# Optimization experiments

Hardware: AMD Instinct MI355X
Metric: run time of the kernel (lower is better)

The kernel has to match this reference:

```python
import jax, jax.numpy as jnp
import numpy as np

D_IN, D_OUT, K = 128, 128, 64
X_MIN, X_MAX = 0.0, 1.0
EPS = 1e-12


def _pchip_slopes(y, x):
    # y: [..., K], x: [K] strictly increasing -> slopes [..., K]. Assumes K >= 3.
    h = x[1:] - x[:-1]                      # [K-1]
    delta = (y[..., 1:] - y[..., :-1]) / (h + EPS)
    h0, h1 = h[:-1], h[1:]
    w1 = 2.0 * h1 + h0
    w2 = h1 + 2.0 * h0
    d0_, d1_ = delta[..., :-1], delta[..., 1:]
    same_sign = d0_ * d1_ > 0
    denom = w1 / (d0_ + EPS) + w2 / (d1_ + EPS)
    d_int = jnp.where(same_sign, (w1 + w2) / (denom + EPS), 0.0)  # [..., K-2]
    d_first = ((2.0 * h[0] + h[1]) * delta[..., 0] - h[0] * delta[..., 1]) / (h[0] + h[1] + EPS)
    d_last = ((2.0 * h[-1] + h[-2]) * delta[..., -1] - h[-1] * delta[..., -2]) / (h[-1] + h[-2] + EPS)

    def limit(di, de):
        di = jnp.where(di * de <= 0, 0.0, di)
        return jnp.where(jnp.abs(di) > 3.0 * jnp.abs(de), 3.0 * de, di)

    d_first = limit(d_first, delta[..., 0])
    d_last = limit(d_last, delta[..., -1])
    return jnp.concatenate([d_first[..., None], d_int, d_last[..., None]], axis=-1)


def setup_inputs() -> dict:
    key = jax.random.key(0)
    k1, k2 = jax.random.split(key)
    x = jax.random.normal(k1, (4096, D_IN), dtype=jnp.float32)
    coeffs = 0.2 * jax.random.normal(k2, (D_OUT, D_IN, K), dtype=jnp.float32)
    bias = jnp.zeros((D_OUT,), dtype=jnp.float32)
    knots = jnp.linspace(X_MIN, X_MAX, K, dtype=jnp.float32)
    return {"x": x, "coeffs": coeffs, "bias": bias, "knots": knots}


def reference(x, coeffs, bias, knots):
    B = x.shape[0]
    slopes = _pchip_slopes(coeffs, knots)              # [d_out, d_in, K]
    h = (X_MAX - X_MIN) / (K - 1)

    xc = jnp.clip(x, X_MIN, X_MAX)                     # [B, d_in]
    idx = jnp.clip(jnp.floor((xc - X_MIN) / h).astype(jnp.int32), 0, K - 2)
    t = (xc - (X_MIN + idx.astype(x.dtype) * h)) / h   # [B, d_in]
    t2 = t * t
    t3 = t2 * t
    h00 = 2 * t3 - 3 * t2 + 1
    h10 = t3 - 2 * t2 + t
    h01 = -2 * t3 + 3 * t2
    h11 = t3 - t2

    ct = jnp.transpose(coeffs, (1, 2, 0))              # [d_in, K, d_out]
    dt = jnp.transpose(slopes, (1, 2, 0))              # [d_in, K, d_out]
    ii = jnp.arange(D_IN)[None, :]                     # [1, d_in]
    y0 = ct[ii, idx]                                   # [B, d_in, d_out]
    y1 = ct[ii, idx + 1]
    d0 = dt[ii, idx]
    d1 = dt[ii, idx + 1]

    yi = (h00[..., None] * y0 + h10[..., None] * h * d0
          + h01[..., None] * y1 + h11[..., None] * h * d1)  # [B, d_in, d_out]

    # linear extrapolation beyond the knot range
    y_left = ct[:, 0, :][None] + dt[:, 0, :][None] * (x - X_MIN)[..., None]
    y_right = ct[:, -1, :][None] + dt[:, -1, :][None] * (x - X_MAX)[..., None]
    yi = jnp.where((x < X_MIN)[..., None], y_left, yi)
    yi = jnp.where((x > X_MAX)[..., None], y_right, yi)

    return yi.sum(axis=1) + bias[None, :]              # [B, d_out]
```

## Files before the change

kernel.cpp:

```cpp
#include <hip/hip_runtime.h>

#define KN 64
#define DIN 128
#define DOUT 128
#define EPSF 1e-12f
#define HF (1.0f / 63.0f)

typedef _Float16 h2 __attribute__((ext_vector_type(2)));
typedef float    f2 __attribute__((ext_vector_type(2)));

#if defined(__has_builtin)
#if __has_builtin(__builtin_amdgcn_fdot2)
#define FDOT2(a, b, c) __builtin_amdgcn_fdot2((a), (b), (c), false)
#endif
#if __has_builtin(__builtin_amdgcn_cvt_pk_fp8_f32) && __has_builtin(__builtin_amdgcn_cvt_pk_f32_fp8)
#define HAVE_HW_FP8 1
#endif
#endif
#ifndef FDOT2
static __device__ __forceinline__ float FDOT2(h2 a, h2 b, float c) {
    return c + (float)a.x * (float)b.x + (float)a.y * (float)b.y;
}
#endif

#ifndef HAVE_HW_FP8
static __device__ __forceinline__ unsigned enc8(float x) {
    unsigned s = (x < 0.0f) ? 1u : 0u;
    x = fabsf(x);
    x = fminf(x, 448.0f);
    if (x < 0.015625f) {
        unsigned m = (unsigned)(x * 512.0f + 0.5f);
        return (s << 7) | m;
    }
    int e; float fr = frexpf(x, &e);
    int E = e - 1 + 7;
    unsigned m = (unsigned)((2.0f * fr - 1.0f) * 8.0f + 0.5f);
    if (m == 8) { m = 0; ++E; }
    if (E > 15) { E = 15; m = 6; }
    return (s << 7) | ((unsigned)E << 3) | m;
}
static __device__ __forceinline__ float dec8(unsigned b) {
    unsigned s = b >> 7, e = (b >> 3) & 15, m = b & 7;
    float v = (e == 0) ? ldexpf((float)m, -9) : ldexpf(8.0f + (float)m, (int)e - 10);
    return s ? -v : v;
}
#endif

static __device__ __forceinline__ unsigned pack4_fp8(float a, float b, float c, float d) {
#ifdef HAVE_HW_FP8
    int r = __builtin_amdgcn_cvt_pk_fp8_f32(a, b, 0, false);
    r = __builtin_amdgcn_cvt_pk_fp8_f32(c, d, r, true);
    return (unsigned)r;
#else
    return enc8(a) | (enc8(b) << 8) | (enc8(c) << 16) | (enc8(d) << 24);
#endif
}
static __device__ __forceinline__ f2 dec2lo(unsigned u) {
#ifdef HAVE_HW_FP8
    return __builtin_amdgcn_cvt_pk_f32_fp8((int)u, false);
#else
    f2 r; r.x = dec8(u & 255u); r.y = dec8((u >> 8) & 255u); return r;
#endif
}
static __device__ __forceinline__ f2 dec2hi(unsigned u) {
#ifdef HAVE_HW_FP8
    return __builtin_amdgcn_cvt_pk_f32_fp8((int)u, true);
#else
    f2 r; r.x = dec8((u >> 16) & 255u); r.y = dec8((u >> 24) & 255u); return r;
#endif
}

#define EXT_ELE (128 * 63 * 64)

__global__ __launch_bounds__(256) void kan_precompute(
    const float* __restrict__ coeffs,
    const float* __restrict__ knots,
    uint2* __restrict__ tb)
{
    const int i      = blockIdx.x >> 1;
    const int o_base = (blockIdx.x & 1) << 6;
    const int wave   = threadIdx.x >> 6;
    const int lane   = threadIdx.x & 63;

    __shared__ float ys[64][65];
    __shared__ float ds[64][65];

    float kn  = knots[lane];
    float kn1 = (lane < 63) ? knots[lane + 1] : 0.0f;
    float hk  = kn1 - kn;
    float hm1 = __shfl_up(hk, 1);
    float h1v = __shfl_down(hk, 1);
    float hm2 = __shfl_up(hk, 2);

    for (int ol = wave; ol < 64; ol += 4) {
        const int o = o_base + ol;
        float y = coeffs[(o * DIN + i) * KN + lane];
        float ynext = __shfl_down(y, 1);
        float delta = (lane < 63) ? (ynext - y) / (hk + EPSF) : 0.0f;
        float dm1 = __shfl_up(delta, 1);

        float w1v = 2.0f * hk + hm1;
        float w2v = hk + 2.0f * hm1;
        float denom = w1v / (dm1 + EPSF) + w2v / (delta + EPSF);
        float d = (dm1 * delta > 0.0f) ? (w1v + w2v) / (denom + EPSF) : 0.0f;

        float d1v = __shfl_down(delta, 1);
        if (lane == 0) {
            float df = ((2.0f * hk + h1v) * delta - hk * d1v) / (hk + h1v + EPSF);
            if (df * delta <= 0.0f) df = 0.0f;
            else if (fabsf(df) > 3.0f * fabsf(delta)) df = 3.0f * delta;
            d = df;
        }
        float dm2 = __shfl_up(delta, 2);
        if (lane == 63) {
            float dl = ((2.0f * hm1 + hm2) * dm1 - hm1 * dm2) / (hm1 + hm2 + EPSF);
            if (dl * dm1 <= 0.0f) dl = 0.0f;
            else if (fabsf(dl) > 3.0f * fabsf(dm1)) dl = 3.0f * dm1;
            d = dl;
        }
        ys[ol][lane] = y;
        ds[ol][lane] = d * HF;
    }
    __syncthreads();

    const int p  = threadIdx.x & 31;
    const int op = (o_base >> 1) + p;
    const int ol0 = p << 1;
    for (int j = threadIdx.x >> 5; j < 63; j += 8) {
        unsigned wa = pack4_fp8(ys[ol0][j],     ds[ol0][j],     ys[ol0][j + 1],     ds[ol0][j + 1]);
        unsigned wb = pack4_fp8(ys[ol0 + 1][j], ds[ol0 + 1][j], ys[ol0 + 1][j + 1], ds[ol0 + 1][j + 1]);
        uint2 v; v.x = wa; v.y = wb;
        tb[(i * 63 + j) * 64 + op] = v;
    }
    if (threadIdx.x < 64) {
        const int pp   = threadIdx.x & 31;
        const int side = threadIdx.x >> 5;
        const int k    = side ? 63 : 0;
        const int o0   = pp << 1;
        h2 ea; ea.x = (_Float16)ys[o0][k];     ea.y = (_Float16)ds[o0][k];
        h2 eb; eb.x = (_Float16)ys[o0 + 1][k]; eb.y = (_Float16)ds[o0 + 1][k];
        uint2 v;
        v.x = __builtin_bit_cast(unsigned int, ea);
        v.y = __builtin_bit_cast(unsigned int, eb);
        tb[EXT_ELE + (i * 2 + side) * 64 + (o_base >> 1) + pp] = v;
    }
}

__global__ __launch_bounds__(256) void kan_main(
    const float* __restrict__ x,
    const uint2* __restrict__ tb2,
    const float* __restrict__ bias,
    float* __restrict__ out)
{
    const int b0   = blockIdx.x << 1;
    const int tid  = threadIdx.x;
    const int wv   = tid >> 6;
    const int bl   = wv >> 1;
    const int half = wv & 1;
    const int lane = tid & 63;

    __shared__ uint4  wl[2][DIN];
    __shared__ float4 wlf[2][DIN];
    __shared__ float2 red[2][64];

    {
        const int bl1 = tid >> 7;
        const int i1  = tid & 127;
        float xv = x[(b0 + bl1) * DIN + i1];
        const bool extL = xv < 0.0f, extR = xv > 1.0f;
        uint4 q; float4 wf;
        if (extL || extR) {
            float tt = extL ? xv * 63.0f : (xv - 1.0f) * 63.0f;
            int side = extL ? 0 : 1;
            h2 w01; w01.x = (_Float16)1.0f; w01.y = (_Float16)tt;
            q.x = __builtin_bit_cast(unsigned int, w01);
            q.y = 0u;
            q.z = (unsigned)(EXT_ELE + ((i1 * 2 + side) << 6));
            q.w = 0u;
            wf = make_float4(0.0f, 0.0f, 0.0f, 0.0f);
        } else {
            int idx = (int)(xv * 63.0f);
            idx = idx > 62 ? 62 : idx;
            float t = xv * 63.0f - (float)idx;
            float t2 = t * t, t3 = t2 * t;
            wf.x = 2.0f * t3 - 3.0f * t2 + 1.0f;
            wf.y = t3 - 2.0f * t2 + t;
            wf.z = 3.0f * t2 - 2.0f * t3;
            wf.w = t3 - t2;
            q.x = 0u; q.y = 0u;
            q.z = (unsigned)((i1 * 63 + idx) << 6);
            q.w = 1u;
        }
        wl[bl1][i1]  = q;
        wlf[bl1][i1] = wf;
    }
    __syncthreads();

    float acc0 = 0.0f, acc1 = 0.0f;
    const int ibase = half << 6;

    #pragma unroll 8
    for (int ii = 0; ii < 64; ++ii) {
        uint4 q = wl[bl][ibase + ii];
        uint2 data = tb2[q.z + (unsigned)lane];
        if (__builtin_amdgcn_readfirstlane((int)q.w)) {
            float4 wf = wlf[bl][ibase + ii];
            f2 l0 = dec2lo(data.x), h0 = dec2hi(data.x);
            f2 l1 = dec2lo(data.y), h1 = dec2hi(data.y);
            acc0 += wf.x * l0.x + wf.y * l0.y + wf.z * h0.x + wf.w * h0.y;
            acc1 += wf.x * l1.x + wf.y * l1.y + wf.z * h1.x + wf.w * h1.y;
        } else {
            h2 w01 = __builtin_bit_cast(h2, q.x);
            acc0 = FDOT2(w01, __builtin_bit_cast(h2, data.x), acc0);
            acc1 = FDOT2(w01, __builtin_bit_cast(h2, data.y), acc1);
        }
    }

    if (half) red[bl][lane] = make_float2(acc0, acc1);
    __syncthreads();
    if (!half) {
        float2 r2 = red[bl][lane];
        const int o0 = lane << 1;
        float2 bo = *reinterpret_cast<const float2*>(&bias[o0]);
        float2 res;
        res.x = acc0 + r2.x + bo.x;
        res.y = acc1 + r2.y + bo.y;
        *reinterpret_cast<float2*>(&out[(b0 + bl) * DOUT + o0]) = res;
    }
}

extern "C" void kernel_launch(void* const* d_in, const int* in_sizes, int n_in,
                              void* d_out, int out_size, void* d_ws, size_t ws_size,
                              hipStream_t stream) {
    const float* x      = (const float*)d_in[0];
    const float* coeffs = (const float*)d_in[1];
    const float* bias   = (const float*)d_in[2];
    const float* knots  = (const float*)d_in[3];
    float* out = (float*)d_out;
    uint2* tb = (uint2*)d_ws;

    kan_precompute<<<256, 256, 0, stream>>>(coeffs, knots, tb);
    kan_main<<<2048, 256, 0, stream>>>(x, tb, bias, out);
}
```

Baseline: 101.0 us.

## Widen table loads to uint4 per lane and split wave across input halves

The lookup table is laid out so each 16-byte uint4 holds four consecutive output channels, and each wave splits into two 32-lane halves that handle different input features. Each lane now accumulates four outputs per 16-byte load instead of two per 8-byte load, halving the loop trip count, and the halves are combined with a cross-lane shuffle. The extrapolation branch is now decided per half-wave rather than via a wave-uniform readfirstlane, so the two halves may diverge and run both paths when they disagree.

```diff
diff --git a/kernel.cpp b/kernel.cpp
--- a/kernel.cpp
+++ b/kernel.cpp
@@ -5,6 +5,9 @@
 #define DOUT 128
 #define EPSF 1e-12f
 #define HF (1.0f / 63.0f)
+
+#define SIDE_ELE (128 * 63 * 32)
+#define SIDE_DW  (128 * 63 * 128)
 
 typedef _Float16 h2 __attribute__((ext_vector_type(2)));
 typedef float    f2 __attribute__((ext_vector_type(2)));
@@ -70,12 +73,11 @@
 #endif
 }
 
-#define EXT_ELE (128 * 63 * 64)
 
 __global__ __launch_bounds__(256) void kan_precompute(
     const float* __restrict__ coeffs,
     const float* __restrict__ knots,
-    uint2* __restrict__ tb)
+    unsigned int* __restrict__ tb)
 {
     const int i      = blockIdx.x >> 1;
     const int o_base = (blockIdx.x & 1) << 6;
@@ -123,32 +125,23 @@
     }
     __syncthreads();
 
-    const int p  = threadIdx.x & 31;
-    const int op = (o_base >> 1) + p;
-    const int ol0 = p << 1;
-    for (int j = threadIdx.x >> 5; j < 63; j += 8) {
-        unsigned wa = pack4_fp8(ys[ol0][j],     ds[ol0][j],     ys[ol0][j + 1],     ds[ol0][j + 1]);
-        unsigned wb = pack4_fp8(ys[ol0 + 1][j], ds[ol0 + 1][j], ys[ol0 + 1][j + 1], ds[ol0 + 1][j + 1]);
-        uint2 v; v.x = wa; v.y = wb;
-        tb[(i * 63 + j) * 64 + op] = v;
-    }
-    if (threadIdx.x < 64) {
-        const int pp   = threadIdx.x & 31;
-        const int side = threadIdx.x >> 5;
+    const int ol = threadIdx.x & 63;
+    const int o  = o_base + ol;
+    for (int j = threadIdx.x >> 6; j < 63; j += 4) {
+        tb[(i * 63 + j) * 128 + o] =
+            pack4_fp8(ys[ol][j], ds[ol][j], ys[ol][j + 1], ds[ol][j + 1]);
+    }
+    if (threadIdx.x < 128) {
+        const int side = threadIdx.x >> 6;
         const int k    = side ? 63 : 0;
-        const int o0   = pp << 1;
-        h2 ea; ea.x = (_Float16)ys[o0][k];     ea.y = (_Float16)ds[o0][k];
-        h2 eb; eb.x = (_Float16)ys[o0 + 1][k]; eb.y = (_Float16)ds[o0 + 1][k];
-        uint2 v;
-        v.x = __builtin_bit_cast(unsigned int, ea);
-        v.y = __builtin_bit_cast(unsigned int, eb);
-        tb[EXT_ELE + (i * 2 + side) * 64 + (o_base >> 1) + pp] = v;
+        h2 v; v.x = (_Float16)ys[ol][k]; v.y = (_Float16)ds[ol][k];
+        tb[SIDE_DW + (i * 2 + side) * 128 + o] = __builtin_bit_cast(unsigned int, v);
     }
 }
 
 __global__ __launch_bounds__(256) void kan_main(
     const float* __restrict__ x,
-    const uint2* __restrict__ tb2,
+    const uint4* __restrict__ tb4,
     const float* __restrict__ bias,
     float* __restrict__ out)
 {
@@ -156,76 +149,89 @@
     const int tid  = threadIdx.x;
     const int wv   = tid >> 6;
     const int bl   = wv >> 1;
-    const int half = wv & 1;
+    const int w2   = wv & 1;
     const int lane = tid & 63;
-
-    __shared__ uint4  wl[2][DIN];
-    __shared__ float4 wlf[2][DIN];
-    __shared__ float2 red[2][64];
+    const int hw   = lane >> 5;
+    const int q32  = lane & 31;
+
+    __shared__ float4 wlw[2][DIN];
+    __shared__ uint2  wlo[2][DIN];
+    __shared__ float4 red[2][32];
 
     {
         const int bl1 = tid >> 7;
         const int i1  = tid & 127;
         float xv = x[(b0 + bl1) * DIN + i1];
-        const bool extL = xv < 0.0f, extR = xv > 1.0f;
-        uint4 q; float4 wf;
-        if (extL || extR) {
-            float tt = extL ? xv * 63.0f : (xv - 1.0f) * 63.0f;
-            int side = extL ? 0 : 1;
-            h2 w01; w01.x = (_Float16)1.0f; w01.y = (_Float16)tt;
-            q.x = __builtin_bit_cast(unsigned int, w01);
-            q.y = 0u;
-            q.z = (unsigned)(EXT_ELE + ((i1 * 2 + side) << 6));
-            q.w = 0u;
-            wf = make_float4(0.0f, 0.0f, 0.0f, 0.0f);
+        float4 w; unsigned base, cls; unsigned w01p = 0;
+        if (xv < 0.0f || xv > 1.0f) {
+            const int side = (xv > 1.0f) ? 1 : 0;
+            float tt = (xv - (side ? 1.0f : 0.0f)) * 63.0f;
+            w = make_float4(1.0f, tt, 0.0f, 0.0f);
+            base = (unsigned)(SIDE_ELE + ((i1 * 2 + side) << 5));
+            cls = 1u;
+            h2 wp; wp.x = (_Float16)1.0f; wp.y = (_Float16)tt;
+            w01p = __builtin_bit_cast(unsigned int, wp);
         } else {
             int idx = (int)(xv * 63.0f);
             idx = idx > 62 ? 62 : idx;
             float t = xv * 63.0f - (float)idx;
             float t2 = t * t, t3 = t2 * t;
-            wf.x = 2.0f * t3 - 3.0f * t2 + 1.0f;
-            wf.y = t3 - 2.0f * t2 + t;
-            wf.z = 3.0f * t2 - 2.0f * t3;
-            wf.w = t3 - t2;
-            q.x = 0u; q.y = 0u;
-            q.z = (unsigned)((i1 * 63 + idx) << 6);
-            q.w = 1u;
-        }
-        wl[bl1][i1]  = q;
-        wlf[bl1][i1] = wf;
+            w.x = 2.0f * t3 - 3.0f * t2 + 1.0f;
+            w.y = t3 - 2.0f * t2 + t;
+            w.z = 3.0f * t2 - 2.0f * t3;
+            w.w = t3 - t2;
+            base = (unsigned)((i1 * 63 + idx) << 5);
+            cls = 0u;
+        }
+        wlw[bl1][i1] = w;
+        uint2 m; m.x = base | (cls << 31); m.y = w01p;
+        wlo[bl1][i1] = m;
     }
     __syncthreads();
 
-    float acc0 = 0.0f, acc1 = 0.0f;
-    const int ibase = half << 6;
+    float4 acc = make_float4(0.0f, 0.0f, 0.0f, 0.0f);
+    const int myib = (w2 << 6) + (hw << 5);
 
     #pragma unroll 8
-    for (int ii = 0; ii < 64; ++ii) {
-        uint4 q = wl[bl][ibase + ii];
-        uint2 data = tb2[q.z + (unsigned)lane];
-        if (__builtin_amdgcn_readfirstlane((int)q.w)) {
-            float4 wf = wlf[bl][ibase + ii];
-            f2 l0 = dec2lo(data.x), h0 = dec2hi(data.x);
-            f2 l1 = dec2lo(data.y), h1 = dec2hi(data.y);
-            acc0 += wf.x * l0.x + wf.y * l0.y + wf.z * h0.x + wf.w * h0.y;
-            acc1 += wf.x * l1.x + wf.y * l1.y + wf.z * h1.x + wf.w * h1.y;
+    for (int n = 0; n < 32; ++n) {
+        float4 w = wlw[bl][myib + n];
+        uint2  m = wlo[bl][myib + n];
+        uint4  r = tb4[(m.x & 0x7FFFFFFFu) + (unsigned)q32];
+        if (m.x >> 31) {
+            h2 w01 = __builtin_bit_cast(h2, m.y);
+            acc.x = FDOT2(w01, __builtin_bit_cast(h2, r.x), acc.x);
+            acc.y = FDOT2(w01, __builtin_bit_cast(h2, r.y), acc.y);
+            acc.z = FDOT2(w01, __builtin_bit_cast(h2, r.z), acc.z);
+            acc.w = FDOT2(w01, __builtin_bit_cast(h2, r.w), acc.w);
         } else {
-            h2 w01 = __builtin_bit_cast(h2, q.x);
-            acc0 = FDOT2(w01, __builtin_bit_cast(h2, data.x), acc0);
-            acc1 = FDOT2(w01, __builtin_bit_cast(h2, data.y), acc1);
-        }
-    }
-
-    if (half) red[bl][lane] = make_float2(acc0, acc1);
+            f2 lo, hi;
+            lo = dec2lo(r.x); hi = dec2hi(r.x);
+            acc.x += w.x * lo.x + w.y * lo.y + w.z * hi.x + w.w * hi.y;
+            lo = dec2lo(r.y); hi = dec2hi(r.y);
+            acc.y += w.x * lo.x + w.y * lo.y + w.z * hi.x + w.w * hi.y;
+            lo = dec2lo(r.z); hi = dec2hi(r.z);
+            acc.z += w.x * lo.x + w.y * lo.y + w.z * hi.x + w.w * hi.y;
+            lo = dec2lo(r.w); hi = dec2hi(r.w);
+            acc.w += w.x * lo.x + w.y * lo.y + w.z * hi.x + w.w * hi.y;
+        }
+    }
+
+    acc.x += __shfl_xor(acc.x, 32);
+    acc.y += __shfl_xor(acc.y, 32);
+    acc.z += __shfl_xor(acc.z, 32);
+    acc.w += __shfl_xor(acc.w, 32);
+
+    if (w2 == 1 && lane < 32) red[bl][q32] = acc;
     __syncthreads();
-    if (!half) {
-        float2 r2 = red[bl][lane];
-        const int o0 = lane << 1;
-        float2 bo = *reinterpret_cast<const float2*>(&bias[o0]);
-        float2 res;
-        res.x = acc0 + r2.x + bo.x;
-        res.y = acc1 + r2.y + bo.y;
-        *reinterpret_cast<float2*>(&out[(b0 + bl) * DOUT + o0]) = res;
+    if (w2 == 0 && lane < 32) {
+        float4 r2 = red[bl][q32];
+        float4 bo = reinterpret_cast<const float4*>(bias)[q32];
+        float4 res;
+        res.x = acc.x + r2.x + bo.x;
+        res.y = acc.y + r2.y + bo.y;
+        res.z = acc.z + r2.z + bo.z;
+        res.w = acc.w + r2.w + bo.w;
+        reinterpret_cast<float4*>(out + (b0 + bl) * DOUT)[q32] = res;
     }
 }
 
@@ -237,8 +243,8 @@
     const float* bias   = (const float*)d_in[2];
     const float* knots  = (const float*)d_in[3];
     float* out = (float*)d_out;
-    uint2* tb = (uint2*)d_ws;
+    unsigned int* tb = (unsigned int*)d_ws;
 
     kan_precompute<<<256, 256, 0, stream>>>(coeffs, knots, tb);
-    kan_main<<<2048, 256, 0, stream>>>(x, tb, bias, out);
-}
+    kan_main<<<2048, 256, 0, stream>>>(x, (const uint4*)tb, bias, out);
+}
```

Result: faster. 94.99 us (-6.0%).
